# Kernel tuning notes

Hardware: AMD Instinct MI355X
Metric: run time of the kernel (lower is better)

Reference implementation:

```python
import jax, jax.numpy as jnp
import numpy as np

B = 16
Dv, Hv, Wv = 128, 128, 128   # patchsize voxel grid (C=1)
NPTS = 1920                  # 16*120 points
EPS_IN = 1e-5                # InstanceNorm eps


def _inorm(x):
    # InstanceNorm1d, affine=False: normalize over last (length) dim per (b, c)
    m = jnp.mean(x, axis=-1, keepdims=True)
    v = jnp.var(x, axis=-1, keepdims=True)
    return (x - m) * jax.lax.rsqrt(v + EPS_IN)


def _mlp(q, w1, b1, w2, b2, w3, b3, w4, b4, w5, b5):
    b = q.shape[0]
    x = q.reshape(b, 256, 8)                                    # (b, 2048//8, 8)
    x = jnp.einsum('bil,oi->bol', x, w1) + b1[None, :, None]    # Conv1d(256,240,1) -> (b,240,8)
    x = jax.nn.relu(_inorm(x.reshape(b, 64, 30)))               # view (b,64,30), IN(64)
    # Conv1d(64,128,1,groups=64): each in-ch -> 2 out-chs; then view (b,32,120)
    x = (x[:, :, None, :] * w2[None, :, :, None] + b2.reshape(1, 64, 2, 1)).reshape(b, 32, 120)
    x = jax.nn.relu(_inorm(x))
    # Conv1d(32,64,1,groups=32); view (b,16,480)
    x = (x[:, :, None, :] * w3[None, :, :, None] + b3.reshape(1, 32, 2, 1)).reshape(b, 16, 480)
    x = jax.nn.relu(_inorm(x))
    # Conv1d(16,64,1,groups=16); view (b,16,1920)
    x = (x[:, :, None, :] * w4[None, :, :, None] + b4.reshape(1, 16, 4, 1)).reshape(b, 16, 1920)
    x = jax.nn.relu(_inorm(x))
    return jnp.einsum('bil,oi->bol', x, w5) + b5[None, :, None]  # Conv1d(16,3,1) -> (b,3,1920)


def _splat(vals, grid):
    # True adjoint of 3D grid_sample (align_corners=False, zeros padding):
    # trilinear scatter-add of point values into the voxel grid.
    # vals: (b, N); grid: (b, N, 3) with (x, y, z) ~ (W, H, D) normalized coords.
    b, n = vals.shape
    px = ((grid[..., 0] + 1.0) * Wv - 1.0) * 0.5
    py = ((grid[..., 1] + 1.0) * Hv - 1.0) * 0.5
    pz = ((grid[..., 2] + 1.0) * Dv - 1.0) * 0.5
    x0f = jnp.floor(px); y0f = jnp.floor(py); z0f = jnp.floor(pz)
    fx = px - x0f; fy = py - y0f; fz = pz - z0f
    x0 = x0f.astype(jnp.int32); y0 = y0f.astype(jnp.int32); z0 = z0f.astype(jnp.int32)
    bidx = jnp.arange(b, dtype=jnp.int32)[:, None]
    out = jnp.zeros(b * Dv * Hv * Wv, dtype=vals.dtype)
    for dz in (0, 1):
        wz = fz if dz else (1.0 - fz)
        for dy in (0, 1):
            wy = fy if dy else (1.0 - fy)
            for dx in (0, 1):
                wx = fx if dx else (1.0 - fx)
                xi = x0 + dx; yi = y0 + dy; zi = z0 + dz
                w = wx * wy * wz * vals
                valid = (xi >= 0) & (xi < Wv) & (yi >= 0) & (yi < Hv) & (zi >= 0) & (zi < Dv)
                w = jnp.where(valid, w, 0.0)
                xi = jnp.clip(xi, 0, Wv - 1)
                yi = jnp.clip(yi, 0, Hv - 1)
                zi = jnp.clip(zi, 0, Dv - 1)
                flat = ((bidx * Dv + zi) * Hv + yi) * Wv + xi
                out = out.at[flat.ravel()].add(w.ravel())
    return out.reshape(b, 1, Dv, Hv, Wv)


def _avgpool3(x):
    # AvgPool3d(3, stride=1, padding=1, count_include_pad=True) as separable 1D averages
    for ax in (2, 3, 4):
        pad = [(1, 1) if i == ax else (0, 0) for i in range(5)]
        xp = jnp.pad(x, pad)
        n = x.shape[ax]
        x = (jax.lax.slice_in_dim(xp, 0, n, axis=ax)
             + jax.lax.slice_in_dim(xp, 1, n + 1, axis=ax)
             + jax.lax.slice_in_dim(xp, 2, n + 2, axis=ax)) / 3.0
    return x


def _smooth(x):
    return _avgpool3(_avgpool3(_avgpool3(x)))


def _forward(q, q_val, w1, b1, w2, b2, w3, b3, w4, b4, w5, b5):
    b = q.shape[0]
    q3 = _mlp(q, w1, b1, w2, b2, w3, b3, w4, b4, w5, b5)   # (b, 3, 1920)
    coords = jnp.tanh(q3)                                    # q0_coord
    grid = jnp.transpose(coords, (0, 2, 1))                  # (b, 1920, 3)
    vals = jnp.broadcast_to(jax.nn.sigmoid(q_val).reshape(1, NPTS), (b, NPTS))
    out = _splat(vals, grid)
    out0 = _splat(jnp.ones((b, NPTS), q.dtype), grid)
    return _smooth(out) / (_smooth(out0) + 0.001)


def setup_inputs() -> dict:
    key = jax.random.key(0)
    ks = jax.random.split(key, 12)
    sc = 0.1
    return {
        'q': jax.random.normal(ks[0], (B, 2048), jnp.float32),
        'q_val': jax.random.normal(ks[1], (1, 1, 16, 120), jnp.float32),
        'w1': jax.random.normal(ks[2], (240, 256), jnp.float32) * sc,
        'b1': jax.random.normal(ks[3], (240,), jnp.float32) * sc,
        'w2': jax.random.normal(ks[4], (64, 2), jnp.float32) * sc,
        'b2': jax.random.normal(ks[5], (128,), jnp.float32) * sc,
        'w3': jax.random.normal(ks[6], (32, 2), jnp.float32) * sc,
        'b3': jax.random.normal(ks[7], (64,), jnp.float32) * sc,
        'w4': jax.random.normal(ks[8], (16, 4), jnp.float32) * sc,
        'b4': jax.random.normal(ks[9], (64,), jnp.float32) * sc,
        'w5': jax.random.normal(ks[10], (3, 16), jnp.float32) * sc,
        'b5': jax.random.normal(ks[11], (3,), jnp.float32) * sc,
    }


def reference(q, q_val, w1, b1, w2, b2, w3, b3, w4, b4, w5, b5):
    return _forward(q, q_val, w1, b1, w2, b2, w3, b3, w4, b4, w5, b5)
```

## Files before the change

### kernel.cpp

```cpp
#include <hip/hip_runtime.h>
#include <cstddef>

#define NB 16
#define NVOX 128
#define NPT 1920

static __device__ __forceinline__ float2 f2(float a, float b) {
    float2 r; r.x = a; r.y = b; return r;
}

__device__ __forceinline__ void coef(int g, float& cm1, float& c0, float& cp1)
{
    cm1 = (g == 1 || g == 127) ? 5.f : 6.f;
    c0  = (g == 0 || g == 127) ? 4.f : 7.f;
    cp1 = (g == 0 || g == 126) ? 5.f : 6.f;
}

__global__ __launch_bounds__(256)
void zero_out(float4* __restrict__ out, int* __restrict__ count)
{
    if (blockIdx.x == 0 && threadIdx.x == 0) *count = 0;
    int idx = blockIdx.x * 2048 + threadIdx.x;
    #pragma unroll
    for (int i = 0; i < 8; ++i)
        out[idx + i * 256] = make_float4(0.f, 0.f, 0.f, 0.f);
}

__global__ __launch_bounds__(1024)
void mega_tail(const float* __restrict__ q, const float* __restrict__ w1,
               const float* __restrict__ b1, const float* __restrict__ qval,
               const float* __restrict__ w2, const float* __restrict__ b2,
               const float* __restrict__ w3, const float* __restrict__ b3,
               const float* __restrict__ w4, const float* __restrict__ b4,
               const float* __restrict__ w5, const float* __restrict__ b5,
               float4* __restrict__ pts, int* __restrict__ count,
               int* __restrict__ list)
{
    __shared__ float x1s[1920];
    __shared__ float h3[7680];
    __shared__ float m4s[16], r4s[16];
    __shared__ unsigned char lflags[2048];

    const int b = blockIdx.x;
    const int t = threadIdx.x;
    float* qs = h3;

    for (int u = t; u < 2048; u += 1024) {
        qs[u] = q[b * 2048 + u];
        lflags[u] = 0;
    }
    __syncthreads();

    for (int u = t; u < 1920; u += 1024) {
        int o = u >> 3, l = u & 7;
        const float4* wr = (const float4*)(w1 + o * 256);
        float acc = 0.f;
        #pragma unroll 8
        for (int i4 = 0; i4 < 64; ++i4) {
            float4 w = wr[i4];
            int base = i4 * 32 + l;
            acc = fmaf(w.x, qs[base],      acc);
            acc = fmaf(w.y, qs[base + 8],  acc);
            acc = fmaf(w.z, qs[base + 16], acc);
            acc = fmaf(w.w, qs[base + 24], acc);
        }
        x1s[u] = b1[o] + acc;
    }
    __syncthreads();

    const int l = t & 63;
    const int c1l = l >> 4;
    const int p16 = l & 15;
    const bool hasb = (p16 < 14);
    {
        const int c3 = t >> 6;
        const int c1 = 4 * c3 + c1l;
        const float* xrow = x1s + c1 * 30;
        float a0 = xrow[p16];
        float a1 = hasb ? xrow[p16 + 16] : 0.f;

        float s = a0 + a1, s2 = a0 * a0 + a1 * a1;
        #pragma unroll
        for (int m = 1; m <= 8; m <<= 1) {
            s  += __shfl_xor(s,  m);
            s2 += __shfl_xor(s2, m);
        }
        float mean = s * (1.f / 30.f);
        float var  = s2 * (1.f / 30.f) - mean * mean;
        float rstd = rsqrtf(var + 1e-5f);
        a0 = fmaxf((a0 - mean) * rstd, 0.f);
        a1 = fmaxf((a1 - mean) * rstd, 0.f);

        const float w20 = w2[c1 * 2 + 0], w21 = w2[c1 * 2 + 1];
        const float b20 = b2[c1 * 2 + 0], b21 = b2[c1 * 2 + 1];
        float y00 = fmaf(a0, w20, b20), y01 = fmaf(a0, w21, b21);
        float y10 = fmaf(a1, w20, b20), y11 = fmaf(a1, w21, b21);

        float u1 = y00 + y01 + (hasb ? (y10 + y11) : 0.f);
        float u2 = y00 * y00 + y01 * y01
                 + (hasb ? (y10 * y10 + y11 * y11) : 0.f);
        #pragma unroll
        for (int m = 1; m <= 16; m <<= 1) {
            u1 += __shfl_xor(u1, m);
            u2 += __shfl_xor(u2, m);
        }
        mean = u1 * (1.f / 120.f);
        var  = u2 * (1.f / 120.f) - mean * mean;
        rstd = rsqrtf(var + 1e-5f);
        y00 = fmaxf((y00 - mean) * rstd, 0.f);
        y01 = fmaxf((y01 - mean) * rstd, 0.f);
        y10 = fmaxf((y10 - mean) * rstd, 0.f);
        y11 = fmaxf((y11 - mean) * rstd, 0.f);

        const int c2 = c1 >> 1;
        const float w30 = w3[c2 * 2 + 0], w31 = w3[c2 * 2 + 1];
        const float b30 = b3[c2 * 2 + 0], b31 = b3[c2 * 2 + 1];
        float z000 = fmaf(y00, w30, b30), z001 = fmaf(y00, w31, b31);
        float z010 = fmaf(y01, w30, b30), z011 = fmaf(y01, w31, b31);
        float z100 = fmaf(y10, w30, b30), z101 = fmaf(y10, w31, b31);
        float z110 = fmaf(y11, w30, b30), z111 = fmaf(y11, w31, b31);

        float v1 = z000 + z001 + z010 + z011
                 + (hasb ? (z100 + z101 + z110 + z111) : 0.f);
        float v2 = z000 * z000 + z001 * z001 + z010 * z010 + z011 * z011
                 + (hasb ? (z100 * z100 + z101 * z101
                          + z110 * z110 + z111 * z111) : 0.f);
        #pragma unroll
        for (int m = 1; m <= 32; m <<= 1) {
            v1 += __shfl_xor(v1, m);
            v2 += __shfl_xor(v2, m);
        }
        mean = v1 * (1.f / 480.f);
        var  = v2 * (1.f / 480.f) - mean * mean;
        rstd = rsqrtf(var + 1e-5f);

        const int qb0 = (c1l >> 1) * 240;
        const int pb0 = (c1l & 1) * 60;
        float* hw = h3 + c3 * 480;
        float s4 = 0.f, q4 = 0.f;
        {
            float v;
            v = fmaxf((z000 - mean) * rstd, 0.f); hw[qb0 +       pb0 +      p16] = v; s4 += v; q4 += v * v;
            v = fmaxf((z001 - mean) * rstd, 0.f); hw[qb0 + 120 + pb0 +      p16] = v; s4 += v; q4 += v * v;
            v = fmaxf((z010 - mean) * rstd, 0.f); hw[qb0 +       pb0 + 30 + p16] = v; s4 += v; q4 += v * v;
            v = fmaxf((z011 - mean) * rstd, 0.f); hw[qb0 + 120 + pb0 + 30 + p16] = v; s4 += v; q4 += v * v;
            if (hasb) {
                v = fmaxf((z100 - mean) * rstd, 0.f); hw[qb0 +       pb0 +      p16 + 16] = v; s4 += v; q4 += v * v;
                v = fmaxf((z101 - mean) * rstd, 0.f); hw[qb0 + 120 + pb0 +      p16 + 16] = v; s4 += v; q4 += v * v;
                v = fmaxf((z110 - mean) * rstd, 0.f); hw[qb0 +       pb0 + 30 + p16 + 16] = v; s4 += v; q4 += v * v;
                v = fmaxf((z111 - mean) * rstd, 0.f); hw[qb0 + 120 + pb0 + 30 + p16 + 16] = v; s4 += v; q4 += v * v;
            }
        }
        #pragma unroll
        for (int m = 1; m <= 32; m <<= 1) {
            s4 += __shfl_xor(s4, m);
            q4 += __shfl_xor(q4, m);
        }
        if (l == 0) {
            float sum4 = 0.f, sq4 = 0.f;
            #pragma unroll
            for (int j = 0; j < 4; ++j) {
                float ww = w4[c3 * 4 + j], bb = b4[c3 * 4 + j];
                sum4 += ww * s4 + 480.f * bb;
                sq4  += ww * ww * q4 + 2.f * ww * bb * s4 + 480.f * bb * bb;
            }
            float m4 = sum4 * (1.f / 1920.f);
            float var4 = sq4 * (1.f / 1920.f) - m4 * m4;
            m4s[c3] = m4; r4s[c3] = rsqrtf(var4 + 1e-5f);
        }
    }
    __syncthreads();

    for (int p = t; p < NPT; p += 1024) {
        int j = p / 480;
        int pp = p - j * 480;
        float a0e = b5[0], a1e = b5[1], a2e = b5[2];
        #pragma unroll
        for (int c = 0; c < 16; ++c) {
            float xv = h3[c * 480 + pp];
            float x4 = fmaf(xv, w4[c * 4 + j], b4[c * 4 + j]);
            float h  = fmaxf((x4 - m4s[c]) * r4s[c], 0.f);
            a0e = fmaf(w5[c],      h, a0e);
            a1e = fmaf(w5[16 + c], h, a1e);
            a2e = fmaf(w5[32 + c], h, a2e);
        }
        float px = tanhf(a0e) * 64.f + 63.5f;
        float py = tanhf(a1e) * 64.f + 63.5f;
        float pz = tanhf(a2e) * 64.f + 63.5f;
        float val = 1.f / (1.f + expf(-qval[p]));

        float4 pv; pv.x = px; pv.y = py; pv.z = pz; pv.w = val;
        pts[b * NPT + p] = pv;

        int x0 = (int)floorf(px), y0 = (int)floorf(py), z0 = (int)floorf(pz);
        int xlo = max(0, x0 - 3), xhi = min(127, x0 + 4);
        int ylo = max(0, y0 - 3), yhi = min(127, y0 + 4);
        int zlo = max(0, z0 - 3), zhi = min(127, z0 + 4);
        if (xlo > xhi || ylo > yhi || zlo > zhi) continue;
        int pxl = xlo >> 4, pxh = xhi >> 4;
        int tyl = ylo >> 3, tyh = yhi >> 3;
        int tzl = zlo >> 3, tzh = zhi >> 3;
        for (int tz = tzl; tz <= tzh; ++tz)
            for (int ty = tyl; ty <= tyh; ++ty)
                for (int px2 = pxl; px2 <= pxh; ++px2)
                    lflags[(tz * 16 + ty) * 8 + px2] = 1;
    }
    __syncthreads();

    for (int u = t; u < 2048; u += 1024) {
        if (lflags[u]) {
            int pos = atomicAdd(count, 1);
            list[pos] = (b << 11) | u;
        }
    }
}

__global__ __launch_bounds__(256, 4)
void tile_persist(const float4* __restrict__ pts, const int* __restrict__ count,
                  const int* __restrict__ list, float* __restrict__ out)
{
    __shared__ float2 raw[4312];

    const int cnt = *count;
    const int t = threadIdx.x;

    for (int idx = blockIdx.x; idx < cnt; idx += gridDim.x) {
        const int code = list[idx];
        const int pair = code & 7;
        const int ty   = (code >> 3) & 15;
        const int tz   = (code >> 7) & 15;
        const int b    = code >> 11;
        const int Tx = pair * 16, Ty = ty * 8, Tz = tz * 8;

        float* ob = out + (((size_t)(b * NVOX + Tz) * NVOX + Ty) * NVOX + Tx);

        {
            float4* rz = (float4*)raw;
            for (int u = t; u < 2156; u += 256) rz[u] = make_float4(0.f, 0.f, 0.f, 0.f);
        }
        __syncthreads();

        const float4* pb = pts + b * NPT;
        for (int p = t; p < NPT; p += 256) {
            float4 pt = pb[p];
            float x0f = floorf(pt.x), y0f = floorf(pt.y), z0f = floorf(pt.z);
            int x0 = (int)x0f, y0 = (int)y0f, z0 = (int)z0f;
            int lx0 = x0 - Tx + 3, ly0 = y0 - Ty + 3, lz0 = z0 - Tz + 3;
            if (lx0 + 1 < 0 || lx0 > 21 || ly0 + 1 < 0 || ly0 > 13 ||
                lz0 + 1 < 0 || lz0 > 13) continue;
            float fx = pt.x - x0f, fy = pt.y - y0f, fz = pt.z - z0f;
            float val = pt.w;
            #pragma unroll
            for (int dz = 0; dz < 2; ++dz) {
                int zi = z0 + dz, lz = lz0 + dz;
                if ((unsigned)zi >= 128u || (unsigned)lz >= 14u) continue;
                float wz = dz ? fz : 1.f - fz;
                #pragma unroll
                for (int dy = 0; dy < 2; ++dy) {
                    int yi = y0 + dy, ly = ly0 + dy;
                    if ((unsigned)yi >= 128u || (unsigned)ly >= 14u) continue;
                    float wy = dy ? fy : 1.f - fy;
                    #pragma unroll
                    for (int dx = 0; dx < 2; ++dx) {
                        int xi = x0 + dx, lx = lx0 + dx;
                        if ((unsigned)xi >= 128u || (unsigned)lx >= 22u) continue;
                        float w = (dx ? fx : 1.f - fx) * wy * wz;
                        float2* cell = &raw[(lz * 14 + ly) * 22 + lx];
                        atomicAdd(&cell->x, w * val);
                        atomicAdd(&cell->y, w);
                    }
                }
            }
        }
        __syncthreads();

        for (int c = t; c < 308; c += 256) {
            float2 w0 = raw[c],            w1_ = raw[c + 308],
                   w2_ = raw[c + 2 * 308], w3_ = raw[c + 3 * 308],
                   w4_ = raw[c + 4 * 308], w5_ = raw[c + 5 * 308],
                   w6_ = raw[c + 6 * 308];
            #pragma unroll
            for (int z = 0; z < 8; ++z) {
                float cm1, c0, cp1; coef(Tz + z, cm1, c0, cp1);
                float sx = (w0.x + w6_.x) + 3.f * (w1_.x + w5_.x)
                         + cm1 * w2_.x + c0 * w3_.x + cp1 * w4_.x;
                float sy = (w0.y + w6_.y) + 3.f * (w1_.y + w5_.y)
                         + cm1 * w2_.y + c0 * w3_.y + cp1 * w4_.y;
                float2 nxt = raw[c + ((z < 7) ? z + 7 : 7) * 308];
                raw[c + z * 308] = f2(sx * (1.f / 27.f), sy * (1.f / 27.f));
                w0 = w1_; w1_ = w2_; w2_ = w3_; w3_ = w4_; w4_ = w5_; w5_ = w6_; w6_ = nxt;
            }
        }
        __syncthreads();

        if (t < 176) {
            int z = t / 22, lx = t - z * 22;
            float2* base = &raw[z * 308 + lx];
            float2 w0 = base[0],       w1_ = base[22],
                   w2_ = base[2 * 22], w3_ = base[3 * 22],
                   w4_ = base[4 * 22], w5_ = base[5 * 22],
                   w6_ = base[6 * 22];
            #pragma unroll
            for (int y = 0; y < 8; ++y) {
                float cm1, c0, cp1; coef(Ty + y, cm1, c0, cp1);
                float sx = (w0.x + w6_.x) + 3.f * (w1_.x + w5_.x)
                         + cm1 * w2_.x + c0 * w3_.x + cp1 * w4_.x;
                float sy = (w0.y + w6_.y) + 3.f * (w1_.y + w5_.y)
                         + cm1 * w2_.y + c0 * w3_.y + cp1 * w4_.y;
                float2 nxt = base[((y < 7) ? y + 7 : 7) * 22];
                base[y * 22] = f2(sx * (1.f / 27.f), sy * (1.f / 27.f));
                w0 = w1_; w1_ = w2_; w2_ = w3_; w3_ = w4_; w4_ = w5_; w5_ = w6_; w6_ = nxt;
            }
        }
        __syncthreads();

        if (t < 128) {
            int row = t >> 1, hx = t & 1;
            int z = row >> 3, y = row & 7;
            const float2* a = &raw[z * 308 + y * 22 + hx * 8];
            float2 w0 = a[0], w1_ = a[1], w2_ = a[2], w3_ = a[3],
                   w4_ = a[4], w5_ = a[5], w6_ = a[6];
            float res[8];
            #pragma unroll
            for (int i = 0; i < 8; ++i) {
                int x = hx * 8 + i;
                float cm1, c0, cp1; coef(Tx + x, cm1, c0, cp1);
                float sx = (w0.x + w6_.x) + 3.f * (w1_.x + w5_.x)
                         + cm1 * w2_.x + c0 * w3_.x + cp1 * w4_.x;
                float sy = (w0.y + w6_.y) + 3.f * (w1_.y + w5_.y)
                         + cm1 * w2_.y + c0 * w3_.y + cp1 * w4_.y;
                res[i] = (sx * (1.f / 27.f)) / (sy * (1.f / 27.f) + 0.001f);
                float2 nxt = a[(i < 7) ? i + 7 : 13];
                w0 = w1_; w1_ = w2_; w2_ = w3_; w3_ = w4_; w4_ = w5_; w5_ = w6_; w6_ = nxt;
            }
            float* orow = &ob[((size_t)z * NVOX + y) * NVOX + hx * 8];
            *(float4*)&orow[0] = make_float4(res[0], res[1], res[2], res[3]);
            *(float4*)&orow[4] = make_float4(res[4], res[5], res[6], res[7]);
        }
        __syncthreads();
    }
}

extern "C" void kernel_launch(void* const* d_in, const int* in_sizes, int n_in,
                              void* d_out, int out_size, void* d_ws, size_t ws_size,
                              hipStream_t stream)
{
    const float* q    = (const float*)d_in[0];
    const float* qval = (const float*)d_in[1];
    const float* w1   = (const float*)d_in[2];
    const float* b1   = (const float*)d_in[3];
    const float* w2   = (const float*)d_in[4];
    const float* b2   = (const float*)d_in[5];
    const float* w3   = (const float*)d_in[6];
    const float* b3   = (const float*)d_in[7];
    const float* w4   = (const float*)d_in[8];
    const float* b4   = (const float*)d_in[9];
    const float* w5   = (const float*)d_in[10];
    const float* b5   = (const float*)d_in[11];
    float* out = (float*)d_out;

    int*    count = (int*)d_ws;
    int*    list  = (int*)((char*)d_ws + 16);
    float4* pts   = (float4*)((char*)d_ws + 131088);

    zero_out<<<4096, 256, 0, stream>>>((float4*)out, count);

    mega_tail<<<NB, 1024, 0, stream>>>(q, w1, b1, qval, w2, b2, w3, b3,
                                       w4, b4, w5, b5, pts, count, list);

    tile_persist<<<2048, 256, 0, stream>>>(pts, count, list, out);
}
```

Baseline: 226.9 us.

## Fuse output zeroing into MLP tail kernel and use per-batch tile lists

Merges the zero-fill kernel into the MLP/point-generation kernel: blocks 0-15 run the per-batch MLP while 496 extra blocks zero the 128 MB output in parallel, removing one launch and overlapping the fill with the MLP. The global atomic counter is replaced by a shared-memory counter per batch, writing to a per-batch list segment and a per-batch count. The splat kernel builds a prefix sum over those counts and maps each work index back to its batch. This adds a small linear search per tile and relies on the extra zeroing blocks sharing the GPU with the 16 MLP blocks.

After: 219.6 us. -3.2%, faster.

```diff
diff --git a/kernel.cpp b/kernel.cpp
--- a/kernel.cpp
+++ b/kernel.cpp
@@ -16,39 +16,41 @@
     cp1 = (g == 0 || g == 126) ? 5.f : 6.f;
 }
 
-__global__ __launch_bounds__(256)
-void zero_out(float4* __restrict__ out, int* __restrict__ count)
+__global__ __launch_bounds__(1024)
+void tail_zero_k(const float* __restrict__ q, const float* __restrict__ w1,
+                 const float* __restrict__ b1, const float* __restrict__ qval,
+                 const float* __restrict__ w2, const float* __restrict__ b2,
+                 const float* __restrict__ w3, const float* __restrict__ b3,
+                 const float* __restrict__ w4, const float* __restrict__ b4,
+                 const float* __restrict__ w5, const float* __restrict__ b5,
+                 float4* __restrict__ pts, int* __restrict__ bcount,
+                 int* __restrict__ list, float4* __restrict__ out4)
 {
-    if (blockIdx.x == 0 && threadIdx.x == 0) *count = 0;
-    int idx = blockIdx.x * 2048 + threadIdx.x;
-    #pragma unroll
-    for (int i = 0; i < 8; ++i)
-        out[idx + i * 256] = make_float4(0.f, 0.f, 0.f, 0.f);
-}
-
-__global__ __launch_bounds__(1024)
-void mega_tail(const float* __restrict__ q, const float* __restrict__ w1,
-               const float* __restrict__ b1, const float* __restrict__ qval,
-               const float* __restrict__ w2, const float* __restrict__ b2,
-               const float* __restrict__ w3, const float* __restrict__ b3,
-               const float* __restrict__ w4, const float* __restrict__ b4,
-               const float* __restrict__ w5, const float* __restrict__ b5,
-               float4* __restrict__ pts, int* __restrict__ count,
-               int* __restrict__ list)
-{
+    const int bid = blockIdx.x;
+    const int t = threadIdx.x;
+
+    if (bid >= NB) {
+        const int stride = 496 * 1024;
+        const int n4 = (NB * NVOX * NVOX * NVOX) / 4;
+        for (int i = (bid - NB) * 1024 + t; i < n4; i += stride)
+            out4[i] = make_float4(0.f, 0.f, 0.f, 0.f);
+        return;
+    }
+
     __shared__ float x1s[1920];
     __shared__ float h3[7680];
     __shared__ float m4s[16], r4s[16];
     __shared__ unsigned char lflags[2048];
-
-    const int b = blockIdx.x;
-    const int t = threadIdx.x;
+    __shared__ int lcount;
+
+    const int b = bid;
     float* qs = h3;
 
     for (int u = t; u < 2048; u += 1024) {
         qs[u] = q[b * 2048 + u];
         lflags[u] = 0;
     }
+    if (t == 0) lcount = 0;
     __syncthreads();
 
     for (int u = t; u < 1920; u += 1024) {
@@ -209,23 +211,38 @@
 
     for (int u = t; u < 2048; u += 1024) {
         if (lflags[u]) {
-            int pos = atomicAdd(count, 1);
-            list[pos] = (b << 11) | u;
-        }
-    }
+            int pos = atomicAdd(&lcount, 1);
+            list[b * 2048 + pos] = (b << 11) | u;
+        }
+    }
+    __syncthreads();
+    if (t == 0) bcount[b] = lcount;
 }
 
 __global__ __launch_bounds__(256, 4)
-void tile_persist(const float4* __restrict__ pts, const int* __restrict__ count,
+void tile_persist(const float4* __restrict__ pts, const int* __restrict__ bcount,
                   const int* __restrict__ list, float* __restrict__ out)
 {
     __shared__ float2 raw[4312];
-
-    const int cnt = *count;
+    __shared__ int pf[17];
+
     const int t = threadIdx.x;
-
-    for (int idx = blockIdx.x; idx < cnt; idx += gridDim.x) {
-        const int code = list[idx];
+    if (t < 16) pf[t + 1] = bcount[t];
+    if (t == 0) pf[0] = 0;
+    __syncthreads();
+    if (t == 0) {
+        int s = 0;
+        #pragma unroll
+        for (int i = 1; i <= 16; ++i) { s += pf[i]; pf[i] = s; }
+    }
+    __syncthreads();
+    const int total = pf[16];
+
+    for (int idx = blockIdx.x; idx < total; idx += gridDim.x) {
+        int bb = 0;
+        #pragma unroll 1
+        for (; bb < 15; ++bb) if (idx < pf[bb + 1]) break;
+        const int code = list[bb * 2048 + (idx - pf[bb])];
         const int pair = code & 7;
         const int ty   = (code >> 3) & 15;
         const int tz   = (code >> 7) & 15;
@@ -359,14 +376,13 @@
     const float* b5   = (const float*)d_in[11];
     float* out = (float*)d_out;
 
-    int*    count = (int*)d_ws;
-    int*    list  = (int*)((char*)d_ws + 16);
-    float4* pts   = (float4*)((char*)d_ws + 131088);
-
-    zero_out<<<4096, 256, 0, stream>>>((float4*)out, count);
-
-    mega_tail<<<NB, 1024, 0, stream>>>(q, w1, b1, qval, w2, b2, w3, b3,
-                                       w4, b4, w5, b5, pts, count, list);
-
-    tile_persist<<<2048, 256, 0, stream>>>(pts, count, list, out);
-}
+    int*    bcount = (int*)d_ws;
+    int*    list   = (int*)((char*)d_ws + 64);
+    float4* pts    = (float4*)((char*)d_ws + 131136);
+
+    tail_zero_k<<<512, 1024, 0, stream>>>(q, w1, b1, qval, w2, b2, w3, b3,
+                                          w4, b4, w5, b5, pts, bcount, list,
+                                          (float4*)out);
+
+    tile_persist<<<2048, 256, 0, stream>>>(pts, bcount, list, out);
+}
```
